# Optimization experiments

Measured on AMD Instinct MI355X. Metric: run time of the kernel, lower is better.

## Reference

```python
import jax, jax.numpy as jnp
import numpy as np

B, S, P, D, H = 2, 1024, 1024, 2048, 16
DH = D // H
QMAX = 127.0


def quantize(x):
    # per-tensor abs-max int8 quantization, matching torch quantize(bits=8)
    scale = jnp.max(jnp.abs(x)) / QMAX
    x_q = jnp.clip(jnp.round(x / scale), -128.0, 127.0).astype(jnp.int8)
    return x_q, scale


def dequantize(x_q, scale):
    return x_q.astype(jnp.float32) * scale


def setup_inputs() -> dict:
    key = jax.random.key(0)
    ks = jax.random.split(key, 12)
    sd = 1.0 / np.sqrt(D)
    inp = {
        'hidden_states': jax.random.normal(ks[0], (B, S, D), jnp.float32),
        'Wq': jax.random.normal(ks[1], (D, D), jnp.float32) * sd,
        'bq': jnp.zeros((D,), jnp.float32),
        'Wk': jax.random.normal(ks[2], (D, D), jnp.float32) * sd,
        'bk': jnp.zeros((D,), jnp.float32),
        'Wv': jax.random.normal(ks[3], (D, D), jnp.float32) * sd,
        'bv': jnp.zeros((D,), jnp.float32),
        'Wo': jax.random.normal(ks[4], (D, D), jnp.float32) * sd,
        'bo': jnp.zeros((D,), jnp.float32),
        'past_k_q': jax.random.randint(ks[5], (B, P, D), -128, 128).astype(jnp.int8),
        'past_k_scale': jnp.float32(0.03),
        'past_v_q': jax.random.randint(ks[6], (B, P, D), -128, 128).astype(jnp.int8),
        'past_v_scale': jnp.float32(0.02),
    }
    return inp


def attention(h, k, v, Wq, bq, Wo, bo):
    # standard causal MHA; query positions are offset by the cache length P
    T = k.shape[1]  # P + S
    q = (h @ Wq + bq).reshape(B, S, H, DH)
    kh = k.reshape(B, T, H, DH)
    vh = v.reshape(B, T, H, DH)
    scores = jnp.einsum('bshd,bthd->bhst', q, kh) / np.sqrt(DH)  # [B,H,S,T]
    causal = jnp.arange(T)[None, :] <= (P + jnp.arange(S))[:, None]  # [S,T]
    scores = jnp.where(causal[None, None], scores, jnp.float32(-1e30))
    attn = jax.nn.softmax(scores, axis=-1)
    out = jnp.einsum('bhst,bthd->bshd', attn, vh).reshape(B, S, D)
    return out @ Wo + bo


def reference(hidden_states, Wq, bq, Wk, bk, Wv, bv, Wo, bo,
              past_k_q, past_k_scale, past_v_q, past_v_scale):
    k = hidden_states @ Wk + bk  # [B,S,D]
    v = hidden_states @ Wv + bv
    k_q, k_scale = quantize(k)
    v_q, v_scale = quantize(v)
    # dequantize cached KV and concat along the sequence dim (dim=1)
    k_prev = dequantize(past_k_q, past_k_scale)
    v_prev = dequantize(past_v_q, past_v_scale)
    k_full = jnp.concatenate([k_prev, k], axis=1)  # [B,P+S,D]
    v_full = jnp.concatenate([v_prev, v], axis=1)
    out = attention(hidden_states, k_full, v_full, Wq, bq, Wo, bo)
    return out, k_q, k_scale, v_q, v_scale
```

## Files before the change

kernel.cpp:

```cpp
#include <hip/hip_runtime.h>

#define SOFT_SCALE 0.08838834764831845f
#define BSD 4194304
#define NELEM 4194304

typedef __attribute__((ext_vector_type(4))) float    f32x4;
typedef __attribute__((ext_vector_type(8))) short    bf16x8;
typedef __attribute__((ext_vector_type(4))) short    bf16x4;
typedef __attribute__((ext_vector_type(4))) unsigned u32x4;

__device__ __forceinline__ float bs2f(short s) {
    unsigned u = ((unsigned)(unsigned short)s) << 16;
    return __builtin_bit_cast(float, u);
}
__device__ __forceinline__ short f2bs(float f) {
    unsigned u = __builtin_bit_cast(unsigned, f);
    unsigned r = (u + 0x7fffu + ((u >> 16) & 1u)) >> 16;
    return (short)r;
}

__device__ __forceinline__ void stage16(const short* g, short* l) {
#if __has_builtin(__builtin_amdgcn_global_load_lds)
    __builtin_amdgcn_global_load_lds(
        (const __attribute__((address_space(1))) void*)g,
        (__attribute__((address_space(3))) void*)l, 16, 0, 0);
#else
    *(bf16x8*)l = *(const bf16x8*)g;
#endif
}

__global__ void probe_init(const int* __restrict__ q, float* __restrict__ scal) {
    const int lane = threadIdx.x;
    int bad = 0;
#pragma unroll
    for (int i = 0; i < 4; ++i) {
        const int v = q[i * 64 + lane];
        bad |= (v < -128 || v > 127) ? 1 : 0;
    }
    const int anybad = __any(bad);
    if (lane == 0) ((int*)scal)[2] = anybad ? 0 : 1;
    if (lane == 1) scal[0] = 0.f;
    if (lane == 2) scal[1] = 0.f;
}

__global__ void conv_bf16(const float* __restrict__ X, short* __restrict__ Y) {
    const int stride = gridDim.x * blockDim.x;
    for (int i = blockIdx.x * blockDim.x + threadIdx.x; i < NELEM / 8; i += stride) {
        const int e = i * 8;
        f32x4 a = *(const f32x4*)&X[e];
        f32x4 b = *(const f32x4*)&X[e + 4];
        bf16x8 o;
        o[0] = f2bs(a[0]); o[1] = f2bs(a[1]); o[2] = f2bs(a[2]); o[3] = f2bs(a[3]);
        o[4] = f2bs(b[0]); o[5] = f2bs(b[1]); o[6] = f2bs(b[2]); o[7] = f2bs(b[3]);
        *(bf16x8*)&Y[e] = o;
    }
}

__global__ __launch_bounds__(256) void transpose_conv(const float* __restrict__ W0,
                                                      const float* __restrict__ W1,
                                                      const float* __restrict__ W2,
                                                      short* __restrict__ WT) {
    __shared__ __align__(16) short Tl[64 * 68];
    const float* W = blockIdx.z == 0 ? W0 : (blockIdx.z == 1 ? W1 : W2);
    short* out = WT + (long)blockIdx.z * 4194304;
    const int tid = threadIdx.x;
    const int n0 = blockIdx.x * 64, k0 = blockIdx.y * 64;
#pragma unroll
    for (int i = 0; i < 4; ++i) {
        const int e = i * 1024 + tid * 4;
        const int r = e >> 6, c = e & 63;
        f32x4 f = *(const f32x4*)&W[(long)(k0 + r) * 2048 + n0 + c];
        bf16x4 s4 = { f2bs(f[0]), f2bs(f[1]), f2bs(f[2]), f2bs(f[3]) };
        *(bf16x4*)&Tl[r * 68 + c] = s4;
    }
    __syncthreads();
#pragma unroll
    for (int i = 0; i < 4; ++i) {
        const int e = i * 1024 + tid * 4;
        const int nr = e >> 6, kk = e & 63;
        bf16x4 o = { Tl[(kk + 0) * 68 + nr], Tl[(kk + 1) * 68 + nr],
                     Tl[(kk + 2) * 68 + nr], Tl[(kk + 3) * 68 + nr] };
        *(bf16x4*)&out[(long)(n0 + nr) * 2048 + k0 + kk] = o;
    }
}

__global__ void dequant_kernel(const void* __restrict__ pk, const void* __restrict__ pv,
                               const float* __restrict__ psk, const float* __restrict__ psv,
                               short* __restrict__ Kf, short* __restrict__ Vf,
                               const int* __restrict__ wsflag) {
    const int z = blockIdx.z;
    const void* src = z ? pv : pk;
    const float sc = z ? *psv : *psk;
    short* dst = z ? Vf : Kf;
    const int flag = wsflag[2];
    const int stride = gridDim.x * blockDim.x;
    for (int i = blockIdx.x * blockDim.x + threadIdx.x; i < NELEM / 8; i += stride) {
        const int e = i * 8;
        int vals[8];
        if (flag) {
            const int* s = (const int*)src + e;
            *(int4*)&vals[0] = *(const int4*)&s[0];
            *(int4*)&vals[4] = *(const int4*)&s[4];
        } else {
            const int2 wv = *(const int2*)((const char*)src + e);
#pragma unroll
            for (int j = 0; j < 4; ++j) vals[j] = (int)(signed char)(wv.x >> (8 * j));
#pragma unroll
            for (int j = 0; j < 4; ++j) vals[4 + j] = (int)(signed char)(wv.y >> (8 * j));
        }
        bf16x8 o;
#pragma unroll
        for (int j = 0; j < 8; ++j) o[j] = f2bs((float)vals[j] * sc);
        *(bf16x8*)&dst[e + ((e >> 21) << 21)] = o;
    }
}

__global__ __launch_bounds__(256, 2) void gemm_m97(
    const short* __restrict__ A,
    const short* __restrict__ Bt0, const short* __restrict__ Bt1, const short* __restrict__ Bt2,
    const float* __restrict__ bi0, const float* __restrict__ bi1, const float* __restrict__ bi2,
    void* __restrict__ o0, void* __restrict__ o1, void* __restrict__ o2,
    float* __restrict__ scal, int mode_sgl, float scale_sgl, int amax_sgl) {
    __shared__ __align__(16) short Al[2][4096];
    __shared__ __align__(16) short Bl[2][4096];
    const int nbx = gridDim.x, nby = gridDim.y, nbz = gridDim.z;
    const int nwg = nbx * nby * nbz;
    const int orig = blockIdx.x + nbx * (blockIdx.y + nby * blockIdx.z);
    const int cpx = nwg >> 3;
    int swz = (orig & 7) * cpx + (orig >> 3);
    const int bx = swz % nbx; swz /= nbx;
    const int by = swz % nby;
    const int bz = swz / nby;

    const short* Bt   = bz == 0 ? Bt0 : (bz == 1 ? Bt1 : Bt2);
    const float* bias = bz == 0 ? bi0 : (bz == 1 ? bi1 : bi2);
    void* outp        = bz == 0 ? o0  : (bz == 1 ? o1  : o2);
    int mode, amx; float scl;
    if (nbz == 3) { mode = (bz == 0) ? 1 : 2; scl = (bz == 0) ? SOFT_SCALE : 1.f;
                    amx = (bz == 0) ? -1 : (bz - 1); }
    else          { mode = mode_sgl; scl = scale_sgl; amx = amax_sgl; }

    const int tid = threadIdx.x, lane = tid & 63, w = tid >> 6;
    const int wm = w >> 1, wn = w & 1, l4 = lane >> 4, ln = lane & 15;
    const int m0 = by * 128, n0 = bx * 128;

    const int srow = tid >> 2;
    const int cswz = ((tid & 3) ^ ((srow >> 1) & 3)) * 8;
    const short* gA0 = A  + (long)(m0 + srow) * 2048 + cswz;
    const short* gA1 = gA0 + 64 * 2048;
    const short* gB0 = Bt + (long)(n0 + srow) * 2048 + cswz;
    const short* gB1 = gB0 + 64 * 2048;

    f32x4 acc[4][4];
#pragma unroll
    for (int mi = 0; mi < 4; ++mi)
#pragma unroll
        for (int ni = 0; ni < 4; ++ni) acc[mi][ni] = (f32x4){0, 0, 0, 0};

#define STAGE_G(buf, ko)                                   \
    do {                                                   \
        stage16(gA0 + (ko), &Al[buf][tid * 8]);            \
        stage16(gA1 + (ko), &Al[buf][2048 + tid * 8]);     \
        stage16(gB0 + (ko), &Bl[buf][tid * 8]);            \
        stage16(gB1 + (ko), &Bl[buf][2048 + tid * 8]);     \
    } while (0)

    STAGE_G(0, 0);
    asm volatile("s_waitcnt vmcnt(0)" ::: "memory");
    __syncthreads();
    int cur = 0;
    const int gsw = (ln >> 1) & 3;
    for (int kt = 0; kt < 64; ++kt) {
        if (kt < 63) STAGE_G(cur ^ 1, (kt + 1) * 32);
        bf16x8 af[4], bfr[4];
#pragma unroll
        for (int mi = 0; mi < 4; ++mi)
            af[mi] = *(const bf16x8*)&Al[cur][(wm * 64 + mi * 16 + ln) * 32 + (l4 ^ gsw) * 8];
#pragma unroll
        for (int ni = 0; ni < 4; ++ni)
            bfr[ni] = *(const bf16x8*)&Bl[cur][(wn * 64 + ni * 16 + ln) * 32 + (l4 ^ gsw) * 8];
#pragma unroll
        for (int mi = 0; mi < 4; ++mi)
#pragma unroll
            for (int ni = 0; ni < 4; ++ni)
                acc[mi][ni] = __builtin_amdgcn_mfma_f32_16x16x32_bf16(
                    af[mi], bfr[ni], acc[mi][ni], 0, 0, 0);
        asm volatile("s_waitcnt vmcnt(0)" ::: "memory");
        __syncthreads();
        cur ^= 1;
    }
#undef STAGE_G

    float amax = 0.f;
#pragma unroll
    for (int ni = 0; ni < 4; ++ni) {
        const int gn = n0 + wn * 64 + ni * 16 + ln;
        const float bv = bias[gn];
#pragma unroll
        for (int mi = 0; mi < 4; ++mi) {
#pragma unroll
            for (int r = 0; r < 4; ++r) {
                const int gm = m0 + wm * 64 + mi * 16 + l4 * 4 + r;
                const float v = (acc[mi][ni][r] + bv) * scl;
                amax = fmaxf(amax, fabsf(v));
                if (mode == 0) {
                    ((float*)outp)[(long)gm * 2048 + gn] = v;
                } else if (mode == 1) {
                    ((short*)outp)[(long)gm * 2048 + gn] = f2bs(v);
                } else {
                    const int gr = gm + 1024 + ((gm >> 10) << 10);
                    ((short*)outp)[(long)gr * 2048 + gn] = f2bs(v);
                }
            }
        }
    }
    if (amx >= 0) {
#pragma unroll
        for (int o = 32; o > 0; o >>= 1) amax = fmaxf(amax, __shfl_xor(amax, o));
        if (lane == 0)
            atomicMax((unsigned int*)&scal[amx], __builtin_bit_cast(unsigned int, amax));
    }
}

__global__ __launch_bounds__(256, 2) void gemm_wo(const short* __restrict__ A,
                                                  const short* __restrict__ Bt,
                                                  const float* __restrict__ bias,
                                                  float* __restrict__ outp) {
    __shared__ __align__(16) short Al[2][4096];
    __shared__ __align__(16) short Bl[2][2048];
    const int orig = blockIdx.x + 32 * blockIdx.y;
    const int swz = (orig & 7) * 64 + (orig >> 3);
    const int bx = swz & 31, by = swz >> 5;
    const int tid = threadIdx.x, lane = tid & 63, w = tid >> 6;
    const int wm = w >> 1, wn = w & 1, l4 = lane >> 4, ln = lane & 15;
    const int m0 = by * 128, n0 = bx * 64;

    const int srow = tid >> 2;
    const int cswz = ((tid & 3) ^ ((srow >> 1) & 3)) * 8;
    const short* gA0 = A  + (long)(m0 + srow) * 2048 + cswz;
    const short* gA1 = gA0 + 64 * 2048;
    const short* gB0 = Bt + (long)(n0 + srow) * 2048 + cswz;

    f32x4 acc[4][2];
#pragma unroll
    for (int mi = 0; mi < 4; ++mi)
#pragma unroll
        for (int ni = 0; ni < 2; ++ni) acc[mi][ni] = (f32x4){0, 0, 0, 0};

#define STAGE_W(buf, ko)                                   \
    do {                                                   \
        stage16(gA0 + (ko), &Al[buf][tid * 8]);            \
        stage16(gA1 + (ko), &Al[buf][2048 + tid * 8]);     \
        stage16(gB0 + (ko), &Bl[buf][tid * 8]);            \
    } while (0)

    STAGE_W(0, 0);
    asm volatile("s_waitcnt vmcnt(0)" ::: "memory");
    __syncthreads();
    int cur = 0;
    const int gsw = (ln >> 1) & 3;
    for (int kt = 0; kt < 64; ++kt) {
        if (kt < 63) STAGE_W(cur ^ 1, (kt + 1) * 32);
        bf16x8 af[4], bfr[2];
#pragma unroll
        for (int mi = 0; mi < 4; ++mi)
            af[mi] = *(const bf16x8*)&Al[cur][(wm * 64 + mi * 16 + ln) * 32 + (l4 ^ gsw) * 8];
#pragma unroll
        for (int ni = 0; ni < 2; ++ni)
            bfr[ni] = *(const bf16x8*)&Bl[cur][(wn * 32 + ni * 16 + ln) * 32 + (l4 ^ gsw) * 8];
#pragma unroll
        for (int mi = 0; mi < 4; ++mi)
#pragma unroll
            for (int ni = 0; ni < 2; ++ni)
                acc[mi][ni] = __builtin_amdgcn_mfma_f32_16x16x32_bf16(
                    af[mi], bfr[ni], acc[mi][ni], 0, 0, 0);
        asm volatile("s_waitcnt vmcnt(0)" ::: "memory");
        __syncthreads();
        cur ^= 1;
    }
#undef STAGE_W

#pragma unroll
    for (int ni = 0; ni < 2; ++ni) {
        const int gn = n0 + wn * 32 + ni * 16 + ln;
        const float bv = bias[gn];
#pragma unroll
        for (int mi = 0; mi < 4; ++mi) {
#pragma unroll
            for (int r = 0; r < 4; ++r) {
                const int gm = m0 + wm * 64 + mi * 16 + l4 * 4 + r;
                outp[(long)gm * 2048 + gn] = acc[mi][ni][r] + bv;
            }
        }
    }
}

__global__ void quantize_kernel(const short* __restrict__ Kf, const short* __restrict__ Vf,
                                const float* __restrict__ scal, float* __restrict__ out) {
    const int z = blockIdx.z;
    const short* src = z ? Vf : Kf;
    const float mx = scal[z];
    const float scale = mx * (1.f / 127.f);
    const float inv = (mx > 0.f) ? 127.f / mx : 0.f;
    const long ob = z ? (2L * BSD + 1) : (1L * BSD);
    if (blockIdx.x == 0 && threadIdx.x == 0)
        out[z ? (3L * BSD + 1) : (2L * BSD)] = scale;
    const int stride = gridDim.x * blockDim.x;
    for (int i = blockIdx.x * blockDim.x + threadIdx.x; i < NELEM / 4; i += stride) {
        const int e = i * 4;
        const int flat = e + 2097152 + ((e >> 21) << 21);
        bf16x4 x4 = *(const bf16x4*)&src[flat];
        float4 q;
        q.x = fminf(127.f, fmaxf(-128.f, rintf(bs2f(x4[0]) * inv)));
        q.y = fminf(127.f, fmaxf(-128.f, rintf(bs2f(x4[1]) * inv)));
        q.z = fminf(127.f, fmaxf(-128.f, rintf(bs2f(x4[2]) * inv)));
        q.w = fminf(127.f, fmaxf(-128.f, rintf(bs2f(x4[3]) * inv)));
        *(float4*)&out[ob + e] = q;
    }
}

__global__ __launch_bounds__(256, 2) void attn_kernel(const short* __restrict__ Q,
                                                      const short* __restrict__ Kf,
                                                      const short* __restrict__ Vf,
                                                      short* __restrict__ O) {
    __shared__ __align__(16) short Kl[64 * 136];
    __shared__ __align__(16) short Vt[128 * 72];
    const int L = blockIdx.x + 16 * (blockIdx.y + 16 * blockIdx.z);
    const int x = L & 7, rr = L >> 3;
    const int qt0 = rr & 15, pgrp = rr >> 4;
    const int p = x + 8 * pgrp;
    const int h = p >> 1, b = p & 1;
    const int qt = (pgrp >= 2) ? (15 - qt0) : qt0;

    const int tid = threadIdx.x, w = tid >> 6, lane = tid & 63;
    const int l4 = lane >> 4, n = lane & 15;
    const int rg = tid >> 4, cg = tid & 15, stc = cg * 8;
    const int sIdx = qt * 64 + w * 16 + n;
    const int qlim = 1024 + sIdx;

    bf16x8 qf[4];
#pragma unroll
    for (int c = 0; c < 4; ++c)
        qf[c] = *(const bf16x8*)&Q[(long)(b * 1024 + sIdx) * 2048 + h * 128 + c * 32 + l4 * 8];

    f32x4 acco[8];
#pragma unroll
    for (int i = 0; i < 8; ++i) acco[i] = (f32x4){0, 0, 0, 0};
    float m_run = -1e30f, l_run = 0.f;

    const short* Kb = Kf + (long)(b * 2048) * 2048 + h * 128;
    const short* Vb = Vf + (long)(b * 2048) * 2048 + h * 128;
    const int nt = 17 + qt;

    bf16x8 kreg[4], vreg[4];
#pragma unroll
    for (int i = 0; i < 4; ++i) kreg[i] = *(const bf16x8*)&Kb[(long)(i * 16 + rg) * 2048 + stc];
#pragma unroll
    for (int i = 0; i < 4; ++i) vreg[i] = *(const bf16x8*)&Vb[(long)(rg * 4 + i) * 2048 + stc];

    for (int t = 0; t < nt; ++t) {
        const int t0 = t * 64;
        __syncthreads();
#pragma unroll
        for (int i = 0; i < 4; ++i)
            *(bf16x8*)&Kl[(i * 16 + rg) * 136 + stc] = kreg[i];
#pragma unroll
        for (int j = 0; j < 8; ++j) {
            const int d = stc + j;
            bf16x4 c4 = { vreg[0][j], vreg[1][j], vreg[2][j], vreg[3][j] };
            *(bf16x4*)&Vt[d * 72 + ((rg ^ ((d >> 3) & 7)) << 2)] = c4;
        }
        if (t + 1 < nt) {
            const int t1 = (t + 1) * 64;
#pragma unroll
            for (int i = 0; i < 4; ++i)
                kreg[i] = *(const bf16x8*)&Kb[(long)(t1 + i * 16 + rg) * 2048 + stc];
#pragma unroll
            for (int i = 0; i < 4; ++i)
                vreg[i] = *(const bf16x8*)&Vb[(long)(t1 + rg * 4 + i) * 2048 + stc];
        }
        __syncthreads();

        float p16[16];
        __builtin_amdgcn_s_setprio(1);
#pragma unroll
        for (int kt = 0; kt < 4; ++kt) {
            f32x4 sc4 = (f32x4){0, 0, 0, 0};
#pragma unroll
            for (int c = 0; c < 4; ++c) {
                bf16x8 kfr = *(const bf16x8*)&Kl[(kt * 16 + n) * 136 + c * 32 + l4 * 8];
                sc4 = __builtin_amdgcn_mfma_f32_16x16x32_bf16(kfr, qf[c], sc4, 0, 0, 0);
            }
#pragma unroll
            for (int r = 0; r < 4; ++r) p16[kt * 4 + r] = sc4[r];
        }
        __builtin_amdgcn_s_setprio(0);
        if (t >= 16) {
#pragma unroll
            for (int i = 0; i < 16; ++i) {
                const int kg = t0 + (i >> 2) * 16 + l4 * 4 + (i & 3);
                if (kg > qlim) p16[i] = -1e30f;
            }
        }

        float tmax = p16[0];
#pragma unroll
        for (int i = 1; i < 16; ++i) tmax = fmaxf(tmax, p16[i]);
        tmax = fmaxf(tmax, __shfl_xor(tmax, 16));
        tmax = fmaxf(tmax, __shfl_xor(tmax, 32));
        if (!__all(tmax <= m_run + 8.f)) {
            const float mnew = fmaxf(m_run, tmax);
            const float fac = __expf(m_run - mnew);
            l_run *= fac;
#pragma unroll
            for (int i = 0; i < 8; ++i) acco[i] *= fac;
            m_run = mnew;
        }
        float tsum = 0.f;
#pragma unroll
        for (int i = 0; i < 16; ++i) { p16[i] = __expf(p16[i] - m_run); tsum += p16[i]; }
        tsum += __shfl_xor(tsum, 16);
        tsum += __shfl_xor(tsum, 32);
        l_run += tsum;

        u32x4 pw0, pw1;
#pragma unroll
        for (int wd = 0; wd < 4; ++wd) {
            unsigned r0, r1;
            asm("v_cvt_pk_bf16_f32 %0, %1, %2" : "=v"(r0) : "v"(p16[2 * wd]), "v"(p16[2 * wd + 1]));
            asm("v_cvt_pk_bf16_f32 %0, %1, %2" : "=v"(r1) : "v"(p16[8 + 2 * wd]), "v"(p16[8 + 2 * wd + 1]));
            pw0[wd] = r0; pw1[wd] = r1;
        }
        bf16x8 pb[2] = { __builtin_bit_cast(bf16x8, pw0), __builtin_bit_cast(bf16x8, pw1) };

        __builtin_amdgcn_s_setprio(1);
#pragma unroll
        for (int dc = 0; dc < 8; ++dc) {
            const int d = dc * 16 + n;
            const int swd = ((d >> 3) & 7) << 2;
#pragma unroll
            for (int k32 = 0; k32 < 2; ++k32) {
                bf16x4 g0 = *(const bf16x4*)&Vt[d * 72 + (k32 * 32 + ((4 * l4) ^ swd))];
                bf16x4 g1 = *(const bf16x4*)&Vt[d * 72 + (k32 * 32 + ((16 + 4 * l4) ^ swd))];
                bf16x8 vf = { g0[0], g0[1], g0[2], g0[3], g1[0], g1[1], g1[2], g1[3] };
                acco[dc] = __builtin_amdgcn_mfma_f32_16x16x32_bf16(vf, pb[k32], acco[dc], 0, 0, 0);
            }
        }
        __builtin_amdgcn_s_setprio(0);
    }

    __syncthreads();
    const float inv = 1.f / l_run;
#pragma unroll
    for (int dc = 0; dc < 8; ++dc)
#pragma unroll
        for (int r = 0; r < 4; ++r)
            Kl[(w * 16 + n) * 136 + dc * 16 + l4 * 4 + r] = f2bs(acco[dc][r] * inv);
    __syncthreads();
#pragma unroll
    for (int i = 0; i < 4; ++i) {
        const int row = i * 4 + (lane >> 4);
        const int col = (lane & 15) * 8;
        bf16x8 ov = *(const bf16x8*)&Kl[(w * 16 + row) * 136 + col];
        *(bf16x8*)&O[(long)(b * 1024 + qt * 64 + w * 16 + row) * 2048 + h * 128 + col] = ov;
    }
}

extern "C" void kernel_launch(void* const* d_in, const int* in_sizes, int n_in,
                              void* d_out, int out_size, void* d_ws, size_t ws_size,
                              hipStream_t stream) {
    const float* h   = (const float*)d_in[0];
    const float* Wq  = (const float*)d_in[1];
    const float* bq  = (const float*)d_in[2];
    const float* Wk  = (const float*)d_in[3];
    const float* bk  = (const float*)d_in[4];
    const float* Wv  = (const float*)d_in[5];
    const float* bv  = (const float*)d_in[6];
    const float* Wo  = (const float*)d_in[7];
    const float* bo  = (const float*)d_in[8];
    const void*  pkq = d_in[9];
    const float* pks = (const float*)d_in[10];
    const void*  pvq = d_in[11];
    const float* pvs = (const float*)d_in[12];
    float* out = (float*)d_out;

    char* ws = (char*)d_ws;
    dim3 blk(256);
    const bool big = (ws_size >= 75500000ull);

    if (big) {
        float* scal  = (float*)ws;
        short* hbf   = (short*)(ws + 256);
        short* WT3   = (short*)(ws + 256 + 1L * 8388608);
        short* Qbf   = (short*)(ws + 256 + 4L * 8388608);
        short* Kfull = (short*)(ws + 256 + 5L * 8388608);
        short* Vfull = (short*)(ws + 256 + 5L * 8388608 + 16777216);
        short* attnb = hbf;

        probe_init<<<1, 64, 0, stream>>>((const int*)pkq, scal);
        conv_bf16<<<1024, blk, 0, stream>>>(h, hbf);
        dequant_kernel<<<dim3(256, 1, 2), blk, 0, stream>>>(pkq, pvq, pks, pvs, Kfull, Vfull,
                                                            (const int*)d_ws);
        transpose_conv<<<dim3(32, 32, 3), blk, 0, stream>>>(Wq, Wk, Wv, WT3);
        gemm_m97<<<dim3(16, 16, 3), blk, 0, stream>>>(hbf, WT3, WT3 + 4194304, WT3 + 8388608,
                                                      bq, bk, bv, Qbf, Kfull, Vfull,
                                                      scal, 0, 1.f, -1);
        quantize_kernel<<<dim3(256, 1, 2), blk, 0, stream>>>(Kfull, Vfull, scal, out);
        attn_kernel<<<dim3(16, 16, 2), blk, 0, stream>>>(Qbf, Kfull, Vfull, attnb);
        transpose_conv<<<dim3(32, 32, 1), blk, 0, stream>>>(Wo, Wo, Wo, WT3);
        gemm_wo<<<dim3(32, 16), blk, 0, stream>>>(attnb, WT3, bo, out);
    } else {
        float* scal  = (float*)ws;
        short* hbf   = (short*)(ws + 256);
        short* WT    = (short*)(ws + 256 + 1L * 8388608);
        short* Qbf   = (short*)(ws + 256 + 2L * 8388608);
        short* Kfull = (short*)(ws + 256 + 3L * 8388608);
        short* Vfull = (short*)(ws + 256 + 3L * 8388608 + 16777216);
        short* attnb = hbf;

        probe_init<<<1, 64, 0, stream>>>((const int*)pkq, scal);
        conv_bf16<<<1024, blk, 0, stream>>>(h, hbf);
        dequant_kernel<<<dim3(256, 1, 2), blk, 0, stream>>>(pkq, pvq, pks, pvs, Kfull, Vfull,
                                                            (const int*)d_ws);
        transpose_conv<<<dim3(32, 32, 1), blk, 0, stream>>>(Wk, Wk, Wk, WT);
        gemm_m97<<<dim3(16, 16, 1), blk, 0, stream>>>(hbf, WT, WT, WT, bk, bk, bk,
                                                      Kfull, Kfull, Kfull, scal, 2, 1.f, 0);
        transpose_conv<<<dim3(32, 32, 1), blk, 0, stream>>>(Wv, Wv, Wv, WT);
        gemm_m97<<<dim3(16, 16, 1), blk, 0, stream>>>(hbf, WT, WT, WT, bv, bv, bv,
                                                      Vfull, Vfull, Vfull, scal, 2, 1.f, 1);
        quantize_kernel<<<dim3(256, 1, 2), blk, 0, stream>>>(Kfull, Vfull, scal, out);
        transpose_conv<<<dim3(32, 32, 1), blk, 0, stream>>>(Wq, Wq, Wq, WT);
        gemm_m97<<<dim3(16, 16, 1), blk, 0, stream>>>(hbf, WT, WT, WT, bq, bq, bq,
                                                      Qbf, Qbf, Qbf, scal, 1, SOFT_SCALE, -1);
        attn_kernel<<<dim3(16, 16, 2), blk, 0, stream>>>(Qbf, Kfull, Vfull, attnb);
        transpose_conv<<<dim3(32, 32, 1), blk, 0, stream>>>(Wo, Wo, Wo, WT);
        gemm_wo<<<dim3(32, 16), blk, 0, stream>>>(attnb, WT, bo, out);
    }
}
```

Baseline: 230.6 us.

## Unfuse absmax from projection GEMMs and drop LDS XOR swizzle

Takes the per-tensor abs-max reduction out of the QKV GEMM epilogue, removing its shuffle reduction and atomicMax, and adds a separate absmax_kernel that re-reads the bf16 K/V tensors before quantization. It also removes the XOR swizzle on the LDS staging and fragment-read addresses in both GEMM kernels. The extra pass adds a kernel launch and about 16 MB of reads. Without the swizzle, the fragment reads, where lanes step through rows 64 bytes apart, may hit LDS bank conflicts.

```diff
diff --git a/kernel.cpp b/kernel.cpp
--- a/kernel.cpp
+++ b/kernel.cpp
@@ -120,7 +120,7 @@
     const short* __restrict__ Bt0, const short* __restrict__ Bt1, const short* __restrict__ Bt2,
     const float* __restrict__ bi0, const float* __restrict__ bi1, const float* __restrict__ bi2,
     void* __restrict__ o0, void* __restrict__ o1, void* __restrict__ o2,
-    float* __restrict__ scal, int mode_sgl, float scale_sgl, int amax_sgl) {
+    int mode_sgl, float scale_sgl) {
     __shared__ __align__(16) short Al[2][4096];
     __shared__ __align__(16) short Bl[2][4096];
     const int nbx = gridDim.x, nby = gridDim.y, nbz = gridDim.z;
@@ -135,20 +135,17 @@
     const short* Bt   = bz == 0 ? Bt0 : (bz == 1 ? Bt1 : Bt2);
     const float* bias = bz == 0 ? bi0 : (bz == 1 ? bi1 : bi2);
     void* outp        = bz == 0 ? o0  : (bz == 1 ? o1  : o2);
-    int mode, amx; float scl;
-    if (nbz == 3) { mode = (bz == 0) ? 1 : 2; scl = (bz == 0) ? SOFT_SCALE : 1.f;
-                    amx = (bz == 0) ? -1 : (bz - 1); }
-    else          { mode = mode_sgl; scl = scale_sgl; amx = amax_sgl; }
+    int mode; float scl;
+    if (nbz == 3) { mode = (bz == 0) ? 1 : 2; scl = (bz == 0) ? SOFT_SCALE : 1.f; }
+    else          { mode = mode_sgl;          scl = scale_sgl; }
 
     const int tid = threadIdx.x, lane = tid & 63, w = tid >> 6;
     const int wm = w >> 1, wn = w & 1, l4 = lane >> 4, ln = lane & 15;
     const int m0 = by * 128, n0 = bx * 128;
 
-    const int srow = tid >> 2;
-    const int cswz = ((tid & 3) ^ ((srow >> 1) & 3)) * 8;
-    const short* gA0 = A  + (long)(m0 + srow) * 2048 + cswz;
+    const short* gA0 = A  + (long)(m0 + (tid >> 2)) * 2048 + (tid & 3) * 8;
     const short* gA1 = gA0 + 64 * 2048;
-    const short* gB0 = Bt + (long)(n0 + srow) * 2048 + cswz;
+    const short* gB0 = Bt + (long)(n0 + (tid >> 2)) * 2048 + (tid & 3) * 8;
     const short* gB1 = gB0 + 64 * 2048;
 
     f32x4 acc[4][4];
@@ -169,16 +166,15 @@
     asm volatile("s_waitcnt vmcnt(0)" ::: "memory");
     __syncthreads();
     int cur = 0;
-    const int gsw = (ln >> 1) & 3;
     for (int kt = 0; kt < 64; ++kt) {
         if (kt < 63) STAGE_G(cur ^ 1, (kt + 1) * 32);
         bf16x8 af[4], bfr[4];
 #pragma unroll
         for (int mi = 0; mi < 4; ++mi)
-            af[mi] = *(const bf16x8*)&Al[cur][(wm * 64 + mi * 16 + ln) * 32 + (l4 ^ gsw) * 8];
+            af[mi] = *(const bf16x8*)&Al[cur][(wm * 64 + mi * 16 + ln) * 32 + l4 * 8];
 #pragma unroll
         for (int ni = 0; ni < 4; ++ni)
-            bfr[ni] = *(const bf16x8*)&Bl[cur][(wn * 64 + ni * 16 + ln) * 32 + (l4 ^ gsw) * 8];
+            bfr[ni] = *(const bf16x8*)&Bl[cur][(wn * 64 + ni * 16 + ln) * 32 + l4 * 8];
 #pragma unroll
         for (int mi = 0; mi < 4; ++mi)
 #pragma unroll
@@ -191,7 +187,6 @@
     }
 #undef STAGE_G
 
-    float amax = 0.f;
 #pragma unroll
     for (int ni = 0; ni < 4; ++ni) {
         const int gn = n0 + wn * 64 + ni * 16 + ln;
@@ -202,7 +197,6 @@
             for (int r = 0; r < 4; ++r) {
                 const int gm = m0 + wm * 64 + mi * 16 + l4 * 4 + r;
                 const float v = (acc[mi][ni][r] + bv) * scl;
-                amax = fmaxf(amax, fabsf(v));
                 if (mode == 0) {
                     ((float*)outp)[(long)gm * 2048 + gn] = v;
                 } else if (mode == 1) {
@@ -213,12 +207,6 @@
                 }
             }
         }
-    }
-    if (amx >= 0) {
-#pragma unroll
-        for (int o = 32; o > 0; o >>= 1) amax = fmaxf(amax, __shfl_xor(amax, o));
-        if (lane == 0)
-            atomicMax((unsigned int*)&scal[amx], __builtin_bit_cast(unsigned int, amax));
     }
 }
 
@@ -235,11 +223,9 @@
     const int wm = w >> 1, wn = w & 1, l4 = lane >> 4, ln = lane & 15;
     const int m0 = by * 128, n0 = bx * 64;
 
-    const int srow = tid >> 2;
-    const int cswz = ((tid & 3) ^ ((srow >> 1) & 3)) * 8;
-    const short* gA0 = A  + (long)(m0 + srow) * 2048 + cswz;
+    const short* gA0 = A  + (long)(m0 + (tid >> 2)) * 2048 + (tid & 3) * 8;
     const short* gA1 = gA0 + 64 * 2048;
-    const short* gB0 = Bt + (long)(n0 + srow) * 2048 + cswz;
+    const short* gB0 = Bt + (long)(n0 + (tid >> 2)) * 2048 + (tid & 3) * 8;
 
     f32x4 acc[4][2];
 #pragma unroll
@@ -258,16 +244,15 @@
     asm volatile("s_waitcnt vmcnt(0)" ::: "memory");
     __syncthreads();
     int cur = 0;
-    const int gsw = (ln >> 1) & 3;
     for (int kt = 0; kt < 64; ++kt) {
         if (kt < 63) STAGE_W(cur ^ 1, (kt + 1) * 32);
         bf16x8 af[4], bfr[2];
 #pragma unroll
         for (int mi = 0; mi < 4; ++mi)
-            af[mi] = *(const bf16x8*)&Al[cur][(wm * 64 + mi * 16 + ln) * 32 + (l4 ^ gsw) * 8];
+            af[mi] = *(const bf16x8*)&Al[cur][(wm * 64 + mi * 16 + ln) * 32 + l4 * 8];
 #pragma unroll
         for (int ni = 0; ni < 2; ++ni)
-            bfr[ni] = *(const bf16x8*)&Bl[cur][(wn * 32 + ni * 16 + ln) * 32 + (l4 ^ gsw) * 8];
+            bfr[ni] = *(const bf16x8*)&Bl[cur][(wn * 32 + ni * 16 + ln) * 32 + l4 * 8];
 #pragma unroll
         for (int mi = 0; mi < 4; ++mi)
 #pragma unroll
@@ -292,6 +277,31 @@
                 outp[(long)gm * 2048 + gn] = acc[mi][ni][r] + bv;
             }
         }
+    }
+}
+
+__global__ void absmax_kernel(const short* __restrict__ Kf, const short* __restrict__ Vf,
+                              float* __restrict__ scal) {
+    const int z = blockIdx.z;
+    const short* src = z ? Vf : Kf;
+    const int tid = threadIdx.x, lane = tid & 63, w = tid >> 6;
+    float mx = 0.f;
+    const int stride = gridDim.x * blockDim.x;
+    for (int i = blockIdx.x * blockDim.x + tid; i < NELEM / 8; i += stride) {
+        const int e = i * 8;
+        const int flat = e + 2097152 + ((e >> 21) << 21);
+        bf16x8 v = *(const bf16x8*)&src[flat];
+#pragma unroll
+        for (int j = 0; j < 8; ++j) mx = fmaxf(mx, fabsf(bs2f(v[j])));
+    }
+#pragma unroll
+    for (int o = 32; o > 0; o >>= 1) mx = fmaxf(mx, __shfl_xor(mx, o));
+    __shared__ float wred[4];
+    if (lane == 0) wred[w] = mx;
+    __syncthreads();
+    if (tid == 0) {
+        const float m2 = fmaxf(fmaxf(wred[0], wred[1]), fmaxf(wred[2], wred[3]));
+        atomicMax((unsigned int*)&scal[z], __builtin_bit_cast(unsigned int, m2));
     }
 }
 
@@ -503,8 +513,8 @@
                                                             (const int*)d_ws);
         transpose_conv<<<dim3(32, 32, 3), blk, 0, stream>>>(Wq, Wk, Wv, WT3);
         gemm_m97<<<dim3(16, 16, 3), blk, 0, stream>>>(hbf, WT3, WT3 + 4194304, WT3 + 8388608,
-                                                      bq, bk, bv, Qbf, Kfull, Vfull,
-                                                      scal, 0, 1.f, -1);
+                                                      bq, bk, bv, Qbf, Kfull, Vfull, 0, 1.f);
+        absmax_kernel<<<dim3(512, 1, 2), blk, 0, stream>>>(Kfull, Vfull, scal);
         quantize_kernel<<<dim3(256, 1, 2), blk, 0, stream>>>(Kfull, Vfull, scal, out);
         attn_kernel<<<dim3(16, 16, 2), blk, 0, stream>>>(Qbf, Kfull, Vfull, attnb);
         transpose_conv<<<dim3(32, 32, 1), blk, 0, stream>>>(Wo, Wo, Wo, WT3);
@@ -524,14 +534,15 @@
                                                             (const int*)d_ws);
         transpose_conv<<<dim3(32, 32, 1), blk, 0, stream>>>(Wk, Wk, Wk, WT);
         gemm_m97<<<dim3(16, 16, 1), blk, 0, stream>>>(hbf, WT, WT, WT, bk, bk, bk,
-                                                      Kfull, Kfull, Kfull, scal, 2, 1.f, 0);
+                                                      Kfull, Kfull, Kfull, 2, 1.f);
         transpose_conv<<<dim3(32, 32, 1), blk, 0, stream>>>(Wv, Wv, Wv, WT);
         gemm_m97<<<dim3(16, 16, 1), blk, 0, stream>>>(hbf, WT, WT, WT, bv, bv, bv,
-                                                      Vfull, Vfull, Vfull, scal, 2, 1.f, 1);
+                                                      Vfull, Vfull, Vfull, 2, 1.f);
+        absmax_kernel<<<dim3(512, 1, 2), blk, 0, stream>>>(Kfull, Vfull, scal);
         quantize_kernel<<<dim3(256, 1, 2), blk, 0, stream>>>(Kfull, Vfull, scal, out);
         transpose_conv<<<dim3(32, 32, 1), blk, 0, stream>>>(Wq, Wq, Wq, WT);
         gemm_m97<<<dim3(16, 16, 1), blk, 0, stream>>>(hbf, WT, WT, WT, bq, bq, bq,
-                                                      Qbf, Qbf, Qbf, scal, 1, SOFT_SCALE, -1);
+                                                      Qbf, Qbf, Qbf, 1, SOFT_SCALE);
         attn_kernel<<<dim3(16, 16, 2), blk, 0, stream>>>(Qbf, Kfull, Vfull, attnb);
         transpose_conv<<<dim3(32, 32, 1), blk, 0, stream>>>(Wo, Wo, Wo, WT);
         gemm_wo<<<dim3(32, 16), blk, 0, stream>>>(attnb, WT, bo, out);
```

Result: no change. 230.5 us (-0.0%).
